# Optimization experiments

Hardware: AMD Instinct MI355X
Metric: run time of the kernel (lower is better)

The kernel has to match this reference:

```python
import jax, jax.numpy as jnp
import numpy as np


def _binarize(x):
    # tf.where(x < 0, -1.0, 1.0)
    return jnp.where(x < 0, -1.0, 1.0).astype(jnp.float32)


def setup_inputs() -> dict:
    key = jax.random.key(0)
    k1, k2, k3 = jax.random.split(key, 3)
    M, K, N = 8192, 2048, 2048
    inputs = jax.random.normal(k1, (M, K), dtype=jnp.float32)
    kernel = jax.random.normal(k2, (K, N), dtype=jnp.float32) * 0.1
    bias = jax.random.normal(k3, (N,), dtype=jnp.float32) * 0.01
    return {"inputs": inputs, "kernel": kernel, "bias": bias}


def reference(inputs, kernel, bias):
    bx = _binarize(inputs)          # [M, K] in {-1, +1}
    bw = _binarize(kernel)          # [K, N] in {-1, +1}
    return jnp.matmul(bx, bw) + bias  # [M, N]
```

## Files before the change

kernel.cpp:

```cpp
#include <hip/hip_runtime.h>
#include <stdint.h>

typedef __attribute__((ext_vector_type(4))) int int4v;
typedef __attribute__((ext_vector_type(8))) int int8v;
typedef __attribute__((ext_vector_type(4))) float floatx4;
typedef __attribute__((ext_vector_type(16))) unsigned char uchar16;

#define MDIM 8192
#define KDIM 2048
#define NDIM 2048
#define BM 128
#define BN 128
#define KB 1024
#define BKB 128

__device__ __forceinline__ void load16_lds(const void* g, void* l) {
  __builtin_amdgcn_global_load_lds(
      (const __attribute__((address_space(1))) void*)g,
      (__attribute__((address_space(3))) void*)l, 16, 0, 0);
}

#define XBLK 2048
#define WBLK 512

__global__ void binarize_fused(const float* __restrict__ X,
                               const float* __restrict__ W,
                               unsigned char* __restrict__ Xb,
                               unsigned char* __restrict__ WbT) {
  const int b = blockIdx.x;
  if (b < XBLK) {
    size_t i = ((size_t)b * 256 + threadIdx.x) * 32;
    const float4* xp = (const float4*)(X + i);
    uchar16 o;
#pragma unroll
    for (int h = 0; h < 8; ++h) {
      float4 a = xp[h];
      unsigned n0 = (a.x < 0.f) ? 0xAu : 0x2u;
      unsigned n1 = (a.y < 0.f) ? 0xAu : 0x2u;
      unsigned n2 = (a.z < 0.f) ? 0xAu : 0x2u;
      unsigned n3 = (a.w < 0.f) ? 0xAu : 0x2u;
      o[2 * h]     = (unsigned char)(n0 | (n1 << 4));
      o[2 * h + 1] = (unsigned char)(n2 | (n3 << 4));
    }
    *(uchar16*)(Xb + i / 2) = o;
  } else {
    const int bw = b - XBLK;
    const int nb = bw & 31;
    const int kb = bw >> 5;
    const int nn = threadIdx.x & 63;
    const int kc = kb * 4 + (threadIdx.x >> 6);
    const float* wp = W + (size_t)(kc * 32) * NDIM + nb * 64 + nn;
    uchar16 o;
#pragma unroll
    for (int j = 0; j < 16; ++j) {
      unsigned lo = (wp[(size_t)(2 * j) * NDIM] < 0.f) ? 0xAu : 0x2u;
      unsigned hi = (wp[(size_t)(2 * j + 1) * NDIM] < 0.f) ? 0xAu : 0x2u;
      o[j] = (unsigned char)(lo | (hi << 4));
    }
    *(uchar16*)(WbT + (size_t)(nb * 64 + nn) * KB + kc * 16) = o;
  }
}

__global__ __launch_bounds__(256) void gemm_bin_fp4(
    const unsigned char* __restrict__ A,
    const unsigned char* __restrict__ B,
    const float* __restrict__ bias,
    float* __restrict__ C) {
  __shared__ __align__(16) unsigned char As[BM * BKB];
  __shared__ __align__(16) unsigned char Bs[BN * BKB];

  const int tid = threadIdx.x;
  const int lane = tid & 63;
  const int wv = tid >> 6;
  const int wm = wv >> 1;
  const int wn = wv & 1;
  const int r = lane & 15;
  const int q = lane >> 4;

  const int m0 = blockIdx.x * BM;
  const int n0 = blockIdx.y * BN;

  floatx4 acc[4][4] = {};

  const int qbase = wv * 256;

  int srcoff[4];
#pragma unroll
  for (int i = 0; i < 4; ++i) {
    const int s = qbase + i * 64 + lane;
    const int row = s >> 3;
    const int cg = (s & 7) ^ (row & 7);
    srcoff[i] = row * KB + cg * 16;
  }

  for (int kb = 0; kb < KB; kb += BKB) {
#pragma unroll
    for (int i = 0; i < 4; ++i) {
      load16_lds(A + (size_t)m0 * KB + kb + srcoff[i],
                 As + (size_t)(qbase + i * 64) * 16);
      load16_lds(B + (size_t)n0 * KB + kb + srcoff[i],
                 Bs + (size_t)(qbase + i * 64) * 16);
    }
    __syncthreads();

#pragma unroll
    for (int s2 = 0; s2 < 2; ++s2) {
      const int cswz = ((s2 * 4 + q) ^ (r & 7)) * 16;
      int8v a8[4], b8[4];
#pragma unroll
      for (int t = 0; t < 4; ++t) {
        int4v av = *(const int4v*)(As + (wm * 64 + t * 16 + r) * BKB + cswz);
        int4v bv = *(const int4v*)(Bs + (wn * 64 + t * 16 + r) * BKB + cswz);
        a8[t] = int8v{av[0], av[1], av[2], av[3], 0, 0, 0, 0};
        b8[t] = int8v{bv[0], bv[1], bv[2], bv[3], 0, 0, 0, 0};
      }
#pragma unroll
      for (int tm = 0; tm < 4; ++tm)
#pragma unroll
        for (int tn = 0; tn < 4; ++tn)
          acc[tm][tn] = __builtin_amdgcn_mfma_scale_f32_16x16x128_f8f6f4(
              a8[tm], b8[tn], acc[tm][tn], 4, 4,
              0, 0x7F7F7F7F, 0, 0x7F7F7F7F);
    }
    __syncthreads();
  }

#pragma unroll
  for (int tn = 0; tn < 4; ++tn) {
    const int col = n0 + wn * 64 + tn * 16 + r;
    const float bv = bias[col];
#pragma unroll
    for (int tm = 0; tm < 4; ++tm) {
      const int rowb = m0 + wm * 64 + tm * 16 + q * 4;
#pragma unroll
      for (int v = 0; v < 4; ++v)
        C[(size_t)(rowb + v) * NDIM + col] = acc[tm][tn][v] + bv;
    }
  }
}

extern "C" void kernel_launch(void* const* d_in, const int* in_sizes, int n_in,
                              void* d_out, int out_size, void* d_ws, size_t ws_size,
                              hipStream_t stream) {
  const float* X = (const float*)d_in[0];
  const float* W = (const float*)d_in[1];
  const float* bias = (const float*)d_in[2];
  float* out = (float*)d_out;

  unsigned char* Xb = (unsigned char*)d_ws;
  unsigned char* WbT = Xb + (size_t)MDIM * KDIM / 2;

  binarize_fused<<<dim3(XBLK + WBLK), 256, 0, stream>>>(X, W, Xb, WbT);
  gemm_bin_fp4<<<dim3(MDIM / BM, NDIM / BN), 256, 0, stream>>>(Xb, WbT, bias, out);
}
```

Before: 146.0 us.

## Double-buffer LDS tiles and enlarge GEMM block to 256x256 with 8 waves

The FP4 GEMM goes from 128x128 tiles with 4 waves to 256x256 tiles with 8 waves, each wave computing a 128x64 sub-tile. The K loop now double-buffers A and B in LDS: it prefetches the next K slice with global_load_lds, then uses explicit vmcnt and lgkmcnt waits and raw barriers instead of __syncthreads, so the loads overlap the MFMA work. A fragments are loaded per tm row to keep register pressure down. The cost is 128KB of LDS per block, which allows only one block per CU and leaves exactly 256 blocks for the whole grid, so there is less latency hiding across blocks and the final wave of blocks is less balanced.

```diff
diff --git a/kernel.cpp b/kernel.cpp
--- a/kernel.cpp
+++ b/kernel.cpp
@@ -9,10 +9,11 @@
 #define MDIM 8192
 #define KDIM 2048
 #define NDIM 2048
-#define BM 128
-#define BN 128
+#define BM 256
+#define BN 256
 #define KB 1024
 #define BKB 128
+#define NT 8
 
 __device__ __forceinline__ void load16_lds(const void* g, void* l) {
   __builtin_amdgcn_global_load_lds(
@@ -61,29 +62,28 @@
   }
 }
 
-__global__ __launch_bounds__(256) void gemm_bin_fp4(
+__global__ __launch_bounds__(512, 2) void gemm_bin_fp4(
     const unsigned char* __restrict__ A,
     const unsigned char* __restrict__ B,
     const float* __restrict__ bias,
     float* __restrict__ C) {
-  __shared__ __align__(16) unsigned char As[BM * BKB];
-  __shared__ __align__(16) unsigned char Bs[BN * BKB];
+  __shared__ __align__(16) unsigned char As[2][BM * BKB];
+  __shared__ __align__(16) unsigned char Bs[2][BN * BKB];
 
   const int tid = threadIdx.x;
   const int lane = tid & 63;
   const int wv = tid >> 6;
-  const int wm = wv >> 1;
-  const int wn = wv & 1;
+  const int wm = wv >> 2;
+  const int wn = wv & 3;
   const int r = lane & 15;
   const int q = lane >> 4;
 
   const int m0 = blockIdx.x * BM;
   const int n0 = blockIdx.y * BN;
 
-  floatx4 acc[4][4] = {};
+  floatx4 acc[8][4] = {};
 
   const int qbase = wv * 256;
-
   int srcoff[4];
 #pragma unroll
   for (int i = 0; i < 4; ++i) {
@@ -92,37 +92,53 @@
     const int cg = (s & 7) ^ (row & 7);
     srcoff[i] = row * KB + cg * 16;
   }
+  const unsigned char* Ab = A + (size_t)m0 * KB;
+  const unsigned char* Bb = B + (size_t)n0 * KB;
 
-  for (int kb = 0; kb < KB; kb += BKB) {
 #pragma unroll
-    for (int i = 0; i < 4; ++i) {
-      load16_lds(A + (size_t)m0 * KB + kb + srcoff[i],
-                 As + (size_t)(qbase + i * 64) * 16);
-      load16_lds(B + (size_t)n0 * KB + kb + srcoff[i],
-                 Bs + (size_t)(qbase + i * 64) * 16);
+  for (int i = 0; i < 4; ++i) {
+    load16_lds(Ab + srcoff[i], &As[0][(qbase + i * 64) * 16]);
+    load16_lds(Bb + srcoff[i], &Bs[0][(qbase + i * 64) * 16]);
+  }
+
+  for (int t = 0; t < NT; ++t) {
+    const int cur = t & 1;
+    if (t < NT - 1) {
+      const int kbb = (t + 1) * BKB;
+#pragma unroll
+      for (int i = 0; i < 4; ++i) {
+        load16_lds(Ab + kbb + srcoff[i], &As[cur ^ 1][(qbase + i * 64) * 16]);
+        load16_lds(Bb + kbb + srcoff[i], &Bs[cur ^ 1][(qbase + i * 64) * 16]);
+      }
+      asm volatile("s_waitcnt vmcnt(8)" ::: "memory");
+    } else {
+      asm volatile("s_waitcnt vmcnt(0)" ::: "memory");
     }
-    __syncthreads();
+    __builtin_amdgcn_s_barrier();
 
 #pragma unroll
     for (int s2 = 0; s2 < 2; ++s2) {
-      const int cswz = ((s2 * 4 + q) ^ (r & 7)) * 16;
-      int8v a8[4], b8[4];
+      int8v b8[4];
 #pragma unroll
-      for (int t = 0; t < 4; ++t) {
-        int4v av = *(const int4v*)(As + (wm * 64 + t * 16 + r) * BKB + cswz);
-        int4v bv = *(const int4v*)(Bs + (wn * 64 + t * 16 + r) * BKB + cswz);
-        a8[t] = int8v{av[0], av[1], av[2], av[3], 0, 0, 0, 0};
-        b8[t] = int8v{bv[0], bv[1], bv[2], bv[3], 0, 0, 0, 0};
+      for (int tn = 0; tn < 4; ++tn) {
+        const int brow = wn * 64 + tn * 16 + r;
+        int4v bv = *(const int4v*)(&Bs[cur][brow * BKB + (((s2 * 4 + q) ^ (r & 7)) * 16)]);
+        b8[tn] = int8v{bv[0], bv[1], bv[2], bv[3], 0, 0, 0, 0};
       }
 #pragma unroll
-      for (int tm = 0; tm < 4; ++tm)
+      for (int tm = 0; tm < 8; ++tm) {
+        const int arow = wm * 128 + tm * 16 + r;
+        int4v av = *(const int4v*)(&As[cur][arow * BKB + (((s2 * 4 + q) ^ (r & 7)) * 16)]);
+        int8v a8 = int8v{av[0], av[1], av[2], av[3], 0, 0, 0, 0};
 #pragma unroll
         for (int tn = 0; tn < 4; ++tn)
           acc[tm][tn] = __builtin_amdgcn_mfma_scale_f32_16x16x128_f8f6f4(
-              a8[tm], b8[tn], acc[tm][tn], 4, 4,
+              a8, b8[tn], acc[tm][tn], 4, 4,
               0, 0x7F7F7F7F, 0, 0x7F7F7F7F);
+      }
     }
-    __syncthreads();
+    asm volatile("s_waitcnt lgkmcnt(0)" ::: "memory");
+    __builtin_amdgcn_s_barrier();
   }
 
 #pragma unroll
@@ -130,8 +146,8 @@
     const int col = n0 + wn * 64 + tn * 16 + r;
     const float bv = bias[col];
 #pragma unroll
-    for (int tm = 0; tm < 4; ++tm) {
-      const int rowb = m0 + wm * 64 + tm * 16 + q * 4;
+    for (int tm = 0; tm < 8; ++tm) {
+      const int rowb = m0 + wm * 128 + tm * 16 + q * 4;
 #pragma unroll
       for (int v = 0; v < 4; ++v)
         C[(size_t)(rowb + v) * NDIM + col] = acc[tm][tn][v] + bv;
@@ -151,5 +167,5 @@
   unsigned char* WbT = Xb + (size_t)MDIM * KDIM / 2;
 
   binarize_fused<<<dim3(XBLK + WBLK), 256, 0, stream>>>(X, W, Xb, WbT);
-  gemm_bin_fp4<<<dim3(MDIM / BM, NDIM / BN), 256, 0, stream>>>(Xb, WbT, bias, out);
+  gemm_bin_fp4<<<dim3(MDIM / BM, NDIM / BN), 512, 0, stream>>>(Xb, WbT, bias, out);
 }
```

Measured after the change: 148.4 us. Within noise of the previous version (+1.7%).
